# Optimization experiments

Measured on AMD Instinct MI355X. Metric: run time of the kernel, lower is better.

The kernel has to match this reference:

```python
import jax, jax.numpy as jnp
import numpy as np

B, S, D, H = 2, 2048, 1024, 16  # batch, pad_size, depth, num_heads
HD = D // H


def setup_inputs() -> dict:
    key = jax.random.key(0)
    ks = jax.random.split(key, 20)
    g = lambda k, shape, fan: jax.random.normal(k, shape, jnp.float32) * np.sqrt(2.0 / fan)
    return {
        "x": jax.random.normal(ks[0], (B, S, D), jnp.float32),
        "W_in": g(ks[1], (D, D), 2 * D), "b_in": g(ks[2], (D,), D),
        "Wq": g(ks[3], (D, D), 2 * D), "bq": g(ks[4], (D,), D),
        "Wk": g(ks[5], (D, D), 2 * D), "bk": g(ks[6], (D,), D),
        "Wv": g(ks[7], (D, D), 2 * D), "bv": g(ks[8], (D,), D),
        "Wo": g(ks[9], (D, D), 2 * D), "bo": g(ks[10], (D,), D),
        "W1": g(ks[11], (D, D), 2 * D), "b1": g(ks[12], (D,), D),
        "W2": g(ks[13], (D, D), 2 * D), "b2": g(ks[14], (D,), D),
        # residual gate scalars (random_id_att / random_id_ff); zero-init in the
        # original, set nonzero here so the whole graph contributes.
        "s_att": jax.random.normal(ks[15], (), jnp.float32),
        "s_ff": jax.random.normal(ks[16], (), jnp.float32),
    }


def reference(x, W_in, b_in, Wq, bq, Wk, bk, Wv, bv, Wo, bo, W1, b1, W2, b2, s_att, s_ff):
    # input projection
    h = x @ W_in + b_in                                   # [B,S,D]
    # QKV projections, split heads -> [B,H,S,HD]
    def heads(t):
        return t.reshape(B, S, H, HD).transpose(0, 2, 1, 3)
    q = heads(h @ Wq + bq)
    k = heads(h @ Wk + bk)
    v = heads(h @ Wv + bv)
    # attention: sigmoid(logits) * tanh(logits) instead of softmax
    logits = jnp.einsum("bhqd,bhkd->bhqk", q, k) / jnp.sqrt(jnp.float32(D))
    attn = jax.nn.sigmoid(logits) * jnp.tanh(logits)      # [B,H,S,S]
    ctx = jnp.einsum("bhqk,bhkd->bhqd", attn, v)
    ctx = ctx.transpose(0, 2, 1, 3).reshape(B, S, D)
    attention = ctx @ Wo + bo
    # gated residual 1
    latent = h + s_att * attention
    # FFN (depth -> depth -> depth), leaky_relu alpha=0.2 (tf default);
    # dropout treated as identity (inference)
    ff = jax.nn.leaky_relu(latent @ W1 + b1, negative_slope=0.2) @ W2 + b2
    out = latent + s_ff * ff
    return out
```

## Files before the change

### kernel.cpp

```cpp
#include <hip/hip_runtime.h>
#include <cstdint>
#include <cstddef>


#define B_ 2
#define S_ 2048
#define D_ 1024
#define H_ 16
#define M_ 4096

typedef __attribute__((ext_vector_type(4))) float  f32x4;
typedef __attribute__((ext_vector_type(8))) __bf16 bf16x8;
typedef __attribute__((ext_vector_type(4))) __bf16 bf16x4;

__device__ __forceinline__ void async16(const void* g, void* l) {
    __builtin_amdgcn_global_load_lds(
        (__attribute__((address_space(1))) void*)(g),
        (__attribute__((address_space(3))) void*)(l), 16, 0, 0);
}

__device__ __forceinline__ float actf(float s) {
    float t = fminf(s * -0.045084223f, 21.6f);
    float u = __builtin_amdgcn_exp2f(t);
    return (1.f - u) * __builtin_amdgcn_rcpf(1.f + u * u);
}

template <int BM, int EPI>
__global__ __launch_bounds__(256) void gemm_k(
    const __bf16* __restrict__ A, const __bf16* __restrict__ Bt,
    const float* __restrict__ bias, const __bf16* __restrict__ aux,
    const float* __restrict__ scal, void* __restrict__ out, int Ntot)
{
    constexpr int K = D_;
    constexpr int MF = BM / 32;
    __shared__ __align__(16) __bf16 As[BM][64];
    __shared__ __align__(16) __bf16 Bs[128][64];

    const int tid = threadIdx.x, wid = tid >> 6, lane = tid & 63;
    const int wr = wid >> 1, wc = wid & 1;
    const int m0 = blockIdx.x * BM, n0 = blockIdx.y * 128;
    const int frow = lane & 15;
    const int kb = (lane >> 4) * 16;
    char* lAs = (char*)As; char* lBs = (char*)Bs;

    f32x4 acc[MF][4] = {};

    for (int k0 = 0; k0 < K; k0 += 64) {
#pragma unroll
        for (int i = 0; i < MF; ++i) {
            const int o = tid * 16 + i * 4096;
            const int row = o >> 7;
            const int cb = (o & 127) ^ ((row & 7) << 4);
            async16(A + (size_t)(m0 + row) * K + k0 + (cb >> 1), lAs + o);
        }
#pragma unroll
        for (int i = 0; i < 4; ++i) {
            const int o = tid * 16 + i * 4096;
            const int row = o >> 7;
            const int cb = (o & 127) ^ ((row & 7) << 4);
            async16(Bt + (size_t)(n0 + row) * K + k0 + (cb >> 1), lBs + o);
        }
        __syncthreads();

#pragma unroll
        for (int kk = 0; kk < 2; ++kk) {
            bf16x8 af[MF], bfr[4];
#pragma unroll
            for (int m = 0; m < MF; ++m) {
                const int r = wr * (BM / 2) + m * 16 + frow;
                af[m] = *(const bf16x8*)(lAs + ((r * 128 + kk * 64 + kb) ^ ((r & 7) << 4)));
            }
#pragma unroll
            for (int n = 0; n < 4; ++n) {
                const int r = wc * 64 + n * 16 + frow;
                bfr[n] = *(const bf16x8*)(lBs + ((r * 128 + kk * 64 + kb) ^ ((r & 7) << 4)));
            }
#pragma unroll
            for (int m = 0; m < MF; ++m)
#pragma unroll
                for (int n = 0; n < 4; ++n)
                    acc[m][n] = __builtin_amdgcn_mfma_f32_16x16x32_bf16(
                        af[m], bfr[n], acc[m][n], 0, 0, 0);
        }
        __syncthreads();
    }

    const float sv = (EPI >= 2) ? *scal : 0.f;
#pragma unroll
    for (int m = 0; m < MF; ++m) {
#pragma unroll
        for (int n = 0; n < 4; ++n) {
#pragma unroll
            for (int r = 0; r < 4; ++r) {
                const int row = m0 + wr * (BM / 2) + m * 16 + (lane >> 4) * 4 + r;
                const int col = n0 + wc * 64 + n * 16 + frow;
                const size_t idx = (size_t)row * Ntot + col;
                float v = acc[m][n][r] + bias[col];
                if constexpr (EPI == 0) {
                    ((__bf16*)out)[idx] = (__bf16)v;
                } else if constexpr (EPI == 1) {
                    v = v > 0.f ? v : 0.2f * v;
                    ((__bf16*)out)[idx] = (__bf16)v;
                } else if constexpr (EPI == 2) {
                    ((__bf16*)out)[idx] = (__bf16)((float)aux[idx] + sv * v);
                } else {
                    ((float*)out)[idx] = (float)aux[idx] + sv * v;
                }
            }
        }
    }
}

__global__ __launch_bounds__(256) void attn_k(
    const __bf16* __restrict__ Q, const __bf16* __restrict__ Kmat,
    const __bf16* __restrict__ VT, __bf16* __restrict__ CTX, int ld)
{
    __shared__ __align__(16) __bf16 Ks[128][64];
    __shared__ __align__(16) __bf16 Vs[64][128];
    __shared__ __align__(16) __bf16 Ps[128][128];

    const int tid = threadIdx.x, wid = tid >> 6, lane = tid & 63;
    const int qt = blockIdx.x, h = blockIdx.y, b = blockIdx.z;
    const int q0 = qt * 128;
    const int frow = lane & 15, kg8 = (lane >> 4) * 8;
    const int kb = kg8 * 2;

    const __bf16* qbase = Q    + (size_t)(b * S_ + q0) * ld + h * 64;
    const __bf16* kbase = Kmat + (size_t)b * S_ * ld + h * 64;
    const __bf16* vbase = VT   + (size_t)(b * H_ + h) * 64 * S_;

    bf16x8 qf[2][2];
#pragma unroll
    for (int m = 0; m < 2; ++m)
#pragma unroll
        for (int kk = 0; kk < 2; ++kk)
            qf[m][kk] = *(const bf16x8*)(qbase +
                (size_t)(wid * 32 + m * 16 + frow) * ld + kk * 32 + kg8);

    f32x4 octx[2][4] = {};
    char* lKs = (char*)Ks; char* lVs = (char*)Vs; char* lPs = (char*)Ps;

    for (int kt = 0; kt < S_; kt += 128) {
        __syncthreads();
#pragma unroll
        for (int i = 0; i < 4; ++i) {
            const int o = (wid * 4 + i) * 1024 + lane * 16;
            {
                const int row = o >> 7;
                const int cb = (o & 127) ^ ((row & 7) << 4);
                async16(kbase + (size_t)(kt + row) * ld + (cb >> 1), lKs + o);
            }
            {
                const int row = o >> 8;
                const int cb = (o & 255) ^ ((row & 7) << 4);
                async16(vbase + (size_t)row * S_ + kt + (cb >> 1), lVs + o);
            }
        }
        __syncthreads();

        f32x4 sacc[2][8] = {};
#pragma unroll
        for (int kk = 0; kk < 2; ++kk) {
            bf16x8 kf[8];
#pragma unroll
            for (int n = 0; n < 8; ++n) {
                const int r = n * 16 + frow;
                kf[n] = *(const bf16x8*)(lKs + ((r * 128 + kk * 64 + kb) ^ ((r & 7) << 4)));
            }
#pragma unroll
            for (int m = 0; m < 2; ++m)
#pragma unroll
                for (int n = 0; n < 8; ++n)
                    sacc[m][n] = __builtin_amdgcn_mfma_f32_16x16x32_bf16(
                        qf[m][kk], kf[n], sacc[m][n], 0, 0, 0);
        }

#pragma unroll
        for (int m = 0; m < 2; ++m)
#pragma unroll
            for (int n = 0; n < 8; ++n)
#pragma unroll
                for (int r = 0; r < 4; ++r) {
                    const float f = actf(sacc[m][n][r]);
                    const int qr = wid * 32 + m * 16 + (lane >> 4) * 4 + r;
                    const int byte = qr * 256 + (n * 16 + frow) * 2;
                    *(__bf16*)(lPs + (byte ^ ((qr & 7) << 4))) = (__bf16)f;
                }

#pragma unroll
        for (int ks = 0; ks < 4; ++ks) {
            bf16x8 pf[2], vf[4];
#pragma unroll
            for (int m = 0; m < 2; ++m) {
                const int r = wid * 32 + m * 16 + frow;
                pf[m] = *(const bf16x8*)(lPs + ((r * 256 + ks * 64 + kb) ^ ((r & 7) << 4)));
            }
#pragma unroll
            for (int n = 0; n < 4; ++n) {
                const int r = n * 16 + frow;
                vf[n] = *(const bf16x8*)(lVs + ((r * 256 + ks * 64 + kb) ^ ((r & 7) << 4)));
            }
#pragma unroll
            for (int m = 0; m < 2; ++m)
#pragma unroll
                for (int n = 0; n < 4; ++n)
                    octx[m][n] = __builtin_amdgcn_mfma_f32_16x16x32_bf16(
                        pf[m], vf[n], octx[m][n], 0, 0, 0);
        }
    }

#pragma unroll
    for (int m = 0; m < 2; ++m)
#pragma unroll
        for (int n = 0; n < 4; ++n)
#pragma unroll
            for (int r = 0; r < 4; ++r) {
                const int row = q0 + wid * 32 + m * 16 + (lane >> 4) * 4 + r;
                const int col = h * 64 + n * 16 + frow;
                CTX[(size_t)(b * S_ + row) * D_ + col] = (__bf16)octx[m][n][r];
            }
}

struct WPack { const float* w[7]; };

__global__ __launch_bounds__(256) void conv_transpose_w(WPack p, __bf16* out) {
    __shared__ float t[32][33];
    const float* W = p.w[blockIdx.z];
    __bf16* o = out + (size_t)blockIdx.z * D_ * D_;
    const int c0 = blockIdx.x * 32, r0 = blockIdx.y * 32;
    const int tx = threadIdx.x, ty = threadIdx.y;
#pragma unroll
    for (int i = 0; i < 4; ++i)
        t[ty + i * 8][tx] = W[(size_t)(r0 + ty + i * 8) * D_ + c0 + tx];
    __syncthreads();
#pragma unroll
    for (int i = 0; i < 4; ++i)
        o[(size_t)(c0 + ty + i * 8) * D_ + r0 + tx] = (__bf16)t[tx][ty + i * 8];
}

__global__ __launch_bounds__(256) void conv_bf16(
    const float* __restrict__ in, __bf16* __restrict__ out, int n4)
{
    const int i = blockIdx.x * blockDim.x + threadIdx.x;
    if (i < n4) {
        f32x4 v = ((const f32x4*)in)[i];
        bf16x4 o;
        o[0] = (__bf16)v[0]; o[1] = (__bf16)v[1];
        o[2] = (__bf16)v[2]; o[3] = (__bf16)v[3];
        ((bf16x4*)out)[i] = o;
    }
}

__global__ __launch_bounds__(256) void bcat_k(
    const float* __restrict__ bq, const float* __restrict__ bk,
    const float* __restrict__ bv, float* __restrict__ o)
{
    const int i = blockIdx.x * 256 + threadIdx.x;
    o[i] = i < 1024 ? bq[i] : (i < 2048 ? bk[i - 1024] : bv[i - 2048]);
}

__global__ __launch_bounds__(256) void transpose_v(
    const __bf16* __restrict__ V, __bf16* __restrict__ VT, int ld)
{
    __shared__ __bf16 t[32][33];
    const int s0 = blockIdx.x * 32, c0 = blockIdx.y * 32, b = blockIdx.z;
    const int tx = threadIdx.x, ty = threadIdx.y;
#pragma unroll
    for (int i = 0; i < 4; ++i)
        t[ty + i * 8][tx] = V[(size_t)(b * S_ + s0 + ty + i * 8) * ld + c0 + tx];
    __syncthreads();
#pragma unroll
    for (int i = 0; i < 4; ++i)
        VT[(size_t)(b * D_ + c0 + ty + i * 8) * S_ + s0 + tx] = t[tx][ty + i * 8];
}

extern "C" void kernel_launch(void* const* d_in, const int* in_sizes, int n_in,
                              void* d_out, int out_size, void* d_ws, size_t ws_size,
                              hipStream_t stream) {
    const float* x    = (const float*)d_in[0];
    const float* W_in = (const float*)d_in[1];
    const float* b_in = (const float*)d_in[2];
    const float* Wq   = (const float*)d_in[3];
    const float* bq   = (const float*)d_in[4];
    const float* Wk   = (const float*)d_in[5];
    const float* bk   = (const float*)d_in[6];
    const float* Wv   = (const float*)d_in[7];
    const float* bv   = (const float*)d_in[8];
    const float* Wo   = (const float*)d_in[9];
    const float* bo   = (const float*)d_in[10];
    const float* W1   = (const float*)d_in[11];
    const float* b1   = (const float*)d_in[12];
    const float* W2   = (const float*)d_in[13];
    const float* b2   = (const float*)d_in[14];
    const float* s_att = (const float*)d_in[15];
    const float* s_ff  = (const float*)d_in[16];

    char* ws = (char*)d_ws;
    const size_t WB = (size_t)D_ * D_ * 2;
    const size_t MB = (size_t)M_ * D_ * 2;
    __bf16* WT   = (__bf16*)(ws);
    __bf16* Hb   = (__bf16*)(ws + 7 * WB);
    __bf16* QKVb = (__bf16*)(ws + 7 * WB + MB);
    __bf16* VTb  = (__bf16*)(ws + 7 * WB + 4 * MB);
    __bf16* Xb   = (__bf16*)(ws + 7 * WB + 5 * MB);
    float*  bcat = (float*)VTb;
    __bf16* CTXb = Xb;
    __bf16* LATb = QKVb;
    __bf16* FF1b = QKVb + (size_t)M_ * D_;
    auto WTi = [&](int i) { return WT + (size_t)i * D_ * D_; };

    WPack wp;
    wp.w[0] = W_in; wp.w[1] = Wq; wp.w[2] = Wk; wp.w[3] = Wv;
    wp.w[4] = Wo;   wp.w[5] = W1; wp.w[6] = W2;
    conv_transpose_w<<<dim3(32, 32, 7), dim3(32, 8), 0, stream>>>(wp, WT);
    conv_bf16<<<dim3(4096), dim3(256), 0, stream>>>(x, Xb, (M_ * D_) / 4);
    bcat_k<<<dim3(12), dim3(256), 0, stream>>>(bq, bk, bv, bcat);

    gemm_k<64, 0><<<dim3(64, 8), dim3(256), 0, stream>>>(
        Xb, WTi(0), b_in, nullptr, nullptr, Hb, D_);
    gemm_k<128, 0><<<dim3(32, 24), dim3(256), 0, stream>>>(
        Hb, WTi(1), bcat, nullptr, nullptr, QKVb, 3 * D_);
    transpose_v<<<dim3(64, 32, 2), dim3(32, 8), 0, stream>>>(
        QKVb + 2 * D_, VTb, 3 * D_);
    attn_k<<<dim3(16, 16, 2), dim3(256), 0, stream>>>(
        QKVb, QKVb + D_, VTb, CTXb, 3 * D_);
    gemm_k<64, 2><<<dim3(64, 8), dim3(256), 0, stream>>>(
        CTXb, WTi(4), bo, Hb, s_att, LATb, D_);
    gemm_k<64, 1><<<dim3(64, 8), dim3(256), 0, stream>>>(
        LATb, WTi(5), b1, nullptr, nullptr, FF1b, D_);
    gemm_k<64, 3><<<dim3(64, 8), dim3(256), 0, stream>>>(
        FF1b, WTi(6), b2, LATb, s_ff, d_out, D_);
}
```

Before: 333.4 us.

## Double-buffer GEMM and attention loads; shrink attention tiles to 64 with transposed scores

The GEMM kernel gets two LDS stages, so the async global-to-LDS load for the next K slice is issued before the MFMA work on the current slice, and one barrier per iteration replaces two. The attention kernel is restructured to 64-query by 64-key tiles with double-buffered K/V staging, which doubles the grid to fill more CUs. It computes K·Qᵀ so each lane holds one query row's scores and can write P as packed 4-element vectors. The intent is to hide load latency and cut barrier stalls, at the cost of more LDS per GEMM block and more K/V tile passes per query in attention.

```diff
diff --git a/kernel.cpp b/kernel.cpp
--- a/kernel.cpp
+++ b/kernel.cpp
@@ -33,47 +33,57 @@
 {
     constexpr int K = D_;
     constexpr int MF = BM / 32;
-    __shared__ __align__(16) __bf16 As[BM][64];
-    __shared__ __align__(16) __bf16 Bs[128][64];
+    __shared__ __align__(16) __bf16 As[2][BM][64];
+    __shared__ __align__(16) __bf16 Bs[2][128][64];
 
     const int tid = threadIdx.x, wid = tid >> 6, lane = tid & 63;
     const int wr = wid >> 1, wc = wid & 1;
     const int m0 = blockIdx.x * BM, n0 = blockIdx.y * 128;
     const int frow = lane & 15;
     const int kb = (lane >> 4) * 16;
-    char* lAs = (char*)As; char* lBs = (char*)Bs;
+    char* cAs = (char*)As; char* cBs = (char*)Bs;
 
     f32x4 acc[MF][4] = {};
 
-    for (int k0 = 0; k0 < K; k0 += 64) {
+    auto stage = [&](int buf, int k0) {
+        char* lA = cAs + buf * (BM * 128);
+        char* lB = cBs + buf * (128 * 128);
 #pragma unroll
         for (int i = 0; i < MF; ++i) {
             const int o = tid * 16 + i * 4096;
             const int row = o >> 7;
             const int cb = (o & 127) ^ ((row & 7) << 4);
-            async16(A + (size_t)(m0 + row) * K + k0 + (cb >> 1), lAs + o);
+            async16(A + (size_t)(m0 + row) * K + k0 + (cb >> 1), lA + o);
         }
 #pragma unroll
         for (int i = 0; i < 4; ++i) {
             const int o = tid * 16 + i * 4096;
             const int row = o >> 7;
             const int cb = (o & 127) ^ ((row & 7) << 4);
-            async16(Bt + (size_t)(n0 + row) * K + k0 + (cb >> 1), lBs + o);
-        }
-        __syncthreads();
-
+            async16(Bt + (size_t)(n0 + row) * K + k0 + (cb >> 1), lB + o);
+        }
+    };
+
+    stage(0, 0);
+    __syncthreads();
+    int cur = 0;
+
+    for (int k0 = 0; k0 < K; k0 += 64) {
+        if (k0 + 64 < K) stage(cur ^ 1, k0 + 64);
+        char* lA = cAs + cur * (BM * 128);
+        char* lB = cBs + cur * (128 * 128);
 #pragma unroll
         for (int kk = 0; kk < 2; ++kk) {
             bf16x8 af[MF], bfr[4];
 #pragma unroll
             for (int m = 0; m < MF; ++m) {
                 const int r = wr * (BM / 2) + m * 16 + frow;
-                af[m] = *(const bf16x8*)(lAs + ((r * 128 + kk * 64 + kb) ^ ((r & 7) << 4)));
+                af[m] = *(const bf16x8*)(lA + ((r * 128 + kk * 64 + kb) ^ ((r & 7) << 4)));
             }
 #pragma unroll
             for (int n = 0; n < 4; ++n) {
                 const int r = wc * 64 + n * 16 + frow;
-                bfr[n] = *(const bf16x8*)(lBs + ((r * 128 + kk * 64 + kb) ^ ((r & 7) << 4)));
+                bfr[n] = *(const bf16x8*)(lB + ((r * 128 + kk * 64 + kb) ^ ((r & 7) << 4)));
             }
 #pragma unroll
             for (int m = 0; m < MF; ++m)
@@ -83,6 +93,7 @@
                         af[m], bfr[n], acc[m][n], 0, 0, 0);
         }
         __syncthreads();
+        cur ^= 1;
     }
 
     const float sv = (EPI >= 2) ? *scal : 0.f;
@@ -111,114 +122,105 @@
     }
 }
 
-__global__ __launch_bounds__(256) void attn_k(
+__global__ __launch_bounds__(256, 4) void attn_k(
     const __bf16* __restrict__ Q, const __bf16* __restrict__ Kmat,
     const __bf16* __restrict__ VT, __bf16* __restrict__ CTX, int ld)
 {
-    __shared__ __align__(16) __bf16 Ks[128][64];
-    __shared__ __align__(16) __bf16 Vs[64][128];
-    __shared__ __align__(16) __bf16 Ps[128][128];
+    __shared__ __align__(16) __bf16 Ks[2][64][64];
+    __shared__ __align__(16) __bf16 Vs[2][64][64];
+    __shared__ __align__(16) __bf16 Ps[64][64];
 
     const int tid = threadIdx.x, wid = tid >> 6, lane = tid & 63;
     const int qt = blockIdx.x, h = blockIdx.y, b = blockIdx.z;
-    const int q0 = qt * 128;
-    const int frow = lane & 15, kg8 = (lane >> 4) * 8;
-    const int kb = kg8 * 2;
+    const int q0 = qt * 64;
+    const int frow = lane & 15, g = lane >> 4;
+    const int kg8 = g * 8, kb = g * 16;
+    const int qrow = wid * 16 + frow;
 
     const __bf16* qbase = Q    + (size_t)(b * S_ + q0) * ld + h * 64;
     const __bf16* kbase = Kmat + (size_t)b * S_ * ld + h * 64;
     const __bf16* vbase = VT   + (size_t)(b * H_ + h) * 64 * S_;
 
-    bf16x8 qf[2][2];
-#pragma unroll
-    for (int m = 0; m < 2; ++m)
-#pragma unroll
-        for (int kk = 0; kk < 2; ++kk)
-            qf[m][kk] = *(const bf16x8*)(qbase +
-                (size_t)(wid * 32 + m * 16 + frow) * ld + kk * 32 + kg8);
-
-    f32x4 octx[2][4] = {};
-    char* lKs = (char*)Ks; char* lVs = (char*)Vs; char* lPs = (char*)Ps;
-
-    for (int kt = 0; kt < S_; kt += 128) {
-        __syncthreads();
-#pragma unroll
-        for (int i = 0; i < 4; ++i) {
-            const int o = (wid * 4 + i) * 1024 + lane * 16;
-            {
-                const int row = o >> 7;
-                const int cb = (o & 127) ^ ((row & 7) << 4);
-                async16(kbase + (size_t)(kt + row) * ld + (cb >> 1), lKs + o);
-            }
-            {
-                const int row = o >> 8;
-                const int cb = (o & 255) ^ ((row & 7) << 4);
-                async16(vbase + (size_t)row * S_ + kt + (cb >> 1), lVs + o);
-            }
-        }
-        __syncthreads();
-
-        f32x4 sacc[2][8] = {};
+    bf16x8 qf[2];
+#pragma unroll
+    for (int kk = 0; kk < 2; ++kk)
+        qf[kk] = *(const bf16x8*)(qbase + (size_t)qrow * ld + kk * 32 + kg8);
+
+    f32x4 octx[4] = {};
+    char* cKs = (char*)Ks; char* cVs = (char*)Vs; char* lPs = (char*)Ps;
+
+    auto stageKV = [&](int buf, int kt) {
+#pragma unroll
+        for (int i = 0; i < 2; ++i) {
+            const int o = tid * 16 + i * 4096;
+            const int row = o >> 7;
+            const int cb = (o & 127) ^ ((row & 7) << 4);
+            async16(kbase + (size_t)(kt + row) * ld + (cb >> 1),
+                    cKs + buf * 8192 + o);
+            async16(vbase + (size_t)row * S_ + kt + (cb >> 1),
+                    cVs + buf * 8192 + o);
+        }
+    };
+
+    stageKV(0, 0);
+    __syncthreads();
+    int cur = 0;
+
+    for (int kt = 0; kt < S_; kt += 64) {
+        if (kt + 64 < S_) stageKV(cur ^ 1, kt + 64);
+        char* lKs = cKs + cur * 8192;
+        char* lVs = cVs + cur * 8192;
+
+        f32x4 scc[4] = {};
 #pragma unroll
         for (int kk = 0; kk < 2; ++kk) {
-            bf16x8 kf[8];
-#pragma unroll
-            for (int n = 0; n < 8; ++n) {
+            bf16x8 kf[4];
+#pragma unroll
+            for (int n = 0; n < 4; ++n) {
                 const int r = n * 16 + frow;
                 kf[n] = *(const bf16x8*)(lKs + ((r * 128 + kk * 64 + kb) ^ ((r & 7) << 4)));
             }
 #pragma unroll
-            for (int m = 0; m < 2; ++m)
-#pragma unroll
-                for (int n = 0; n < 8; ++n)
-                    sacc[m][n] = __builtin_amdgcn_mfma_f32_16x16x32_bf16(
-                        qf[m][kk], kf[n], sacc[m][n], 0, 0, 0);
-        }
-
-#pragma unroll
-        for (int m = 0; m < 2; ++m)
-#pragma unroll
-            for (int n = 0; n < 8; ++n)
-#pragma unroll
-                for (int r = 0; r < 4; ++r) {
-                    const float f = actf(sacc[m][n][r]);
-                    const int qr = wid * 32 + m * 16 + (lane >> 4) * 4 + r;
-                    const int byte = qr * 256 + (n * 16 + frow) * 2;
-                    *(__bf16*)(lPs + (byte ^ ((qr & 7) << 4))) = (__bf16)f;
-                }
-
-#pragma unroll
-        for (int ks = 0; ks < 4; ++ks) {
-            bf16x8 pf[2], vf[4];
-#pragma unroll
-            for (int m = 0; m < 2; ++m) {
-                const int r = wid * 32 + m * 16 + frow;
-                pf[m] = *(const bf16x8*)(lPs + ((r * 256 + ks * 64 + kb) ^ ((r & 7) << 4)));
-            }
-#pragma unroll
-            for (int n = 0; n < 4; ++n) {
-                const int r = n * 16 + frow;
-                vf[n] = *(const bf16x8*)(lVs + ((r * 256 + ks * 64 + kb) ^ ((r & 7) << 4)));
-            }
-#pragma unroll
-            for (int m = 0; m < 2; ++m)
-#pragma unroll
-                for (int n = 0; n < 4; ++n)
-                    octx[m][n] = __builtin_amdgcn_mfma_f32_16x16x32_bf16(
-                        pf[m], vf[n], octx[m][n], 0, 0, 0);
-        }
+            for (int n = 0; n < 4; ++n)
+                scc[n] = __builtin_amdgcn_mfma_f32_16x16x32_bf16(
+                    kf[n], qf[kk], scc[n], 0, 0, 0);
+        }
+
+#pragma unroll
+        for (int n = 0; n < 4; ++n) {
+            bf16x4 pw;
+#pragma unroll
+            for (int r = 0; r < 4; ++r) pw[r] = (__bf16)actf(scc[n][r]);
+            *(bf16x4*)(lPs + ((qrow * 128 + n * 32 + g * 8) ^ ((qrow & 7) << 4))) = pw;
+        }
+
+#pragma unroll
+        for (int ks = 0; ks < 2; ++ks) {
+            bf16x8 pf = *(const bf16x8*)(lPs +
+                ((qrow * 128 + ks * 64 + kb) ^ ((qrow & 7) << 4)));
+            bf16x8 vf[4];
+#pragma unroll
+            for (int nd = 0; nd < 4; ++nd) {
+                const int rd = nd * 16 + frow;
+                vf[nd] = *(const bf16x8*)(lVs + ((rd * 128 + ks * 64 + kb) ^ ((rd & 7) << 4)));
+            }
+#pragma unroll
+            for (int nd = 0; nd < 4; ++nd)
+                octx[nd] = __builtin_amdgcn_mfma_f32_16x16x32_bf16(
+                    pf, vf[nd], octx[nd], 0, 0, 0);
+        }
+        __syncthreads();
+        cur ^= 1;
     }
 
 #pragma unroll
-    for (int m = 0; m < 2; ++m)
-#pragma unroll
-        for (int n = 0; n < 4; ++n)
-#pragma unroll
-            for (int r = 0; r < 4; ++r) {
-                const int row = q0 + wid * 32 + m * 16 + (lane >> 4) * 4 + r;
-                const int col = h * 64 + n * 16 + frow;
-                CTX[(size_t)(b * S_ + row) * D_ + col] = (__bf16)octx[m][n][r];
-            }
+    for (int nd = 0; nd < 4; ++nd)
+#pragma unroll
+        for (int r = 0; r < 4; ++r) {
+            const int row = q0 + wid * 16 + g * 4 + r;
+            const int col = h * 64 + nd * 16 + frow;
+            CTX[(size_t)(b * S_ + row) * D_ + col] = (__bf16)octx[nd][r];
+        }
 }
 
 struct WPack { const float* w[7]; };
@@ -322,7 +324,7 @@
         Hb, WTi(1), bcat, nullptr, nullptr, QKVb, 3 * D_);
     transpose_v<<<dim3(64, 32, 2), dim3(32, 8), 0, stream>>>(
         QKVb + 2 * D_, VTb, 3 * D_);
-    attn_k<<<dim3(16, 16, 2), dim3(256), 0, stream>>>(
+    attn_k<<<dim3(32, 16, 2), dim3(256), 0, stream>>>(
         QKVb, QKVb + D_, VTb, CTXb, 3 * D_);
     gemm_k<64, 2><<<dim3(64, 8), dim3(256), 0, stream>>>(
         CTXb, WTi(4), bo, Hb, s_att, LATb, D_);
```

After: 299.0 us. -10.3%, faster.
